# Performance work log

Measured on AMD Instinct MI355X. Metric: run time of the kernel, lower is better.

## Reference

```python
import jax, jax.numpy as jnp
import numpy as np

EMBED = 1024
HEADS = 16
HEAD_DIM = EMBED // HEADS

def setup_inputs() -> dict:
    key = jax.random.key(0)
    ks = jax.random.split(key, 5)
    B, S = 2, 2048
    scale = 1.0 / np.sqrt(EMBED)
    return {
        "query": jax.random.normal(ks[0], (B, S, EMBED), dtype=jnp.float32),
        "w_qkv": jax.random.normal(ks[1], (3 * EMBED, EMBED), dtype=jnp.float32) * scale,
        "b_qkv": jax.random.normal(ks[2], (3 * EMBED,), dtype=jnp.float32) * 0.01,
        "w_out": jax.random.normal(ks[3], (EMBED, EMBED), dtype=jnp.float32) * scale,
        "b_out": jax.random.normal(ks[4], (EMBED,), dtype=jnp.float32) * 0.01,
    }

def reference(query, w_qkv, b_qkv, w_out, b_out):
    B, S, E = query.shape
    H, D = HEADS, HEAD_DIM
    # fused qkv projection (torch Linear: x @ W.T + b)
    qkv = query @ w_qkv.T + b_qkv          # [B, S, 3E]
    q, k, v = jnp.split(qkv, 3, axis=-1)   # each [B, S, E]
    def heads(x):
        return x.reshape(B, S, H, D).transpose(0, 2, 1, 3)  # [B, H, S, D]
    q, k, v = heads(q), heads(k), heads(v)
    scale = D ** -0.5
    energy = jnp.einsum('bhqd,bhkd->bhqk', q, k) * scale    # [B, H, S, S]
    attn = jax.nn.softmax(energy, axis=-1)
    # dropout: inference mode (identity)
    out = jnp.einsum('bhqk,bhkd->bhqd', attn, v)            # [B, H, S, D]
    out = out.transpose(0, 2, 1, 3).reshape(B, S, E)
    return out @ w_out.T + b_out
```

## Files before the change

### kernel.cpp

```cpp
#include <hip/hip_runtime.h>
#include <hip/hip_bf16.h>
#include <cstdint>
#include <cstddef>


typedef float f32x4  __attribute__((ext_vector_type(4)));
typedef float f32x16 __attribute__((ext_vector_type(16)));
typedef short s16x8  __attribute__((ext_vector_type(8)));

#define AS1C(p) ((const __attribute__((address_space(1))) void*)(p))
#define AS3(p)  ((__attribute__((address_space(3))) void*)(p))

__device__ __forceinline__ unsigned short f2bf(float f) {
    union { float f; unsigned u; } v; v.f = f;
    return (unsigned short)((v.u + 0x7FFFu + ((v.u >> 16) & 1u)) >> 16);
}

__device__ __forceinline__ float fast_exp2(float x) {
#if __has_builtin(__builtin_amdgcn_exp2f)
    return __builtin_amdgcn_exp2f(x);
#else
    return exp2f(x);
#endif
}

__device__ __forceinline__ float fast_rcp(float x) {
#if __has_builtin(__builtin_amdgcn_rcpf)
    return __builtin_amdgcn_rcpf(x);
#else
    return 1.0f / x;
#endif
}

__device__ __forceinline__ unsigned pk_bf2(float lo, float hi) {
    __hip_bfloat162 p = __float22bfloat162_rn(make_float2(lo, hi));
    return *(unsigned*)&p;
}

__global__ void cvt_bf16_3(const float* __restrict__ a, const float* __restrict__ b,
                           const float* __restrict__ c,
                           unsigned short* __restrict__ oa, unsigned short* __restrict__ ob,
                           unsigned short* __restrict__ oc,
                           int na4, int nb4, int nc4) {
    int j = blockIdx.x * blockDim.x + threadIdx.x;
    const float* s; unsigned short* d;
    if (j < na4) { s = a; d = oa; }
    else {
        j -= na4;
        if (j < nb4) { s = b; d = ob; }
        else { j -= nb4; if (j >= nc4) return; s = c; d = oc; }
    }
    float4 f = reinterpret_cast<const float4*>(s)[j];
    ushort4 o;
    o.x = f2bf(f.x); o.y = f2bf(f.y); o.z = f2bf(f.z); o.w = f2bf(f.w);
    reinterpret_cast<ushort4*>(d)[j] = o;
}

#define QSCALE_L2E (0.125f * 1.44269504088896f)

template <int MODE>
__global__ __launch_bounds__(256, 2)
void gemm_bt(const unsigned short* __restrict__ A,
             const unsigned short* __restrict__ B,
             const float* __restrict__ bias,
             float* __restrict__ Cf,
             unsigned short* __restrict__ Qw,
             unsigned short* __restrict__ Kw,
             unsigned short* __restrict__ Vtw,
             int M, int N, int K) {
    constexpr int BK = 32;
    __shared__ unsigned short As[128 * BK];
    __shared__ unsigned short Bs[128 * BK];

    const int tid = threadIdx.x;
    const int wid = tid >> 6, lane = tid & 63;
    const int brow = blockIdx.y * 128, bcol = blockIdx.x * 128;
    const int wr = wid >> 1, wc = wid & 1;

    f32x4 acc[4][4] = {};

    const int kIters = K / BK;
    for (int kt = 0; kt < kIters; ++kt) {
#pragma unroll
        for (int i = 0; i < 2; ++i) {
            const int lb = (wid * 2 + i) * 1024;
            const int row = (lb >> 6) + (lane >> 2);
            const int inrow = (lane & 3) * 16;
            const char* ga = (const char*)A + ((size_t)(brow + row) * K + kt * BK) * 2 + inrow;
            __builtin_amdgcn_global_load_lds(AS1C(ga), AS3((char*)As + lb), 16, 0, 0);
            const char* gb = (const char*)B + ((size_t)(bcol + row) * K + kt * BK) * 2 + inrow;
            __builtin_amdgcn_global_load_lds(AS1C(gb), AS3((char*)Bs + lb), 16, 0, 0);
        }
        __syncthreads();

        s16x8 af[4], bfr[4];
#pragma unroll
        for (int f = 0; f < 4; ++f) {
            af[f]  = *(const s16x8*)((const char*)As + (wr * 64 + f * 16 + (lane & 15)) * 64 + (lane >> 4) * 16);
            bfr[f] = *(const s16x8*)((const char*)Bs + (wc * 64 + f * 16 + (lane & 15)) * 64 + (lane >> 4) * 16);
        }
#pragma unroll
        for (int mf = 0; mf < 4; ++mf)
#pragma unroll
            for (int nf = 0; nf < 4; ++nf)
                acc[mf][nf] = __builtin_amdgcn_mfma_f32_16x16x32_bf16(af[mf], bfr[nf], acc[mf][nf], 0, 0, 0);
        __syncthreads();
    }

    float bv[4];
#pragma unroll
    for (int nf = 0; nf < 4; ++nf) bv[nf] = bias[bcol + wc * 64 + nf * 16 + (lane & 15)];

#pragma unroll
    for (int mf = 0; mf < 4; ++mf) {
#pragma unroll
        for (int r = 0; r < 4; ++r) {
            const int row = brow + wr * 64 + mf * 16 + (lane >> 4) * 4 + r;
#pragma unroll
            for (int nf = 0; nf < 4; ++nf) {
                const int col = bcol + wc * 64 + nf * 16 + (lane & 15);
                float v = acc[mf][nf][r] + bv[nf];
                if constexpr (MODE == 0) {
                    const int which = col >> 10, e = col & 1023;
                    const int h = e >> 6, d = e & 63;
                    const int b = row >> 11, s = row & 2047;
                    const size_t bh = (size_t)(b * 16 + h);
                    if (which == 0)      Qw[(bh * 2048 + s) * 64 + d] = f2bf(v * QSCALE_L2E);
                    else if (which == 1) Kw[(bh * 2048 + s) * 64 + d] = f2bf(v);
                    else                 Vtw[(bh * 64 + d) * 2048 + s] = f2bf(v);
                } else {
                    Cf[(size_t)row * N + col] = v;
                }
            }
        }
    }
}

__global__ __launch_bounds__(128, 2)
void attn_fwd(const unsigned short* __restrict__ Q,
              const unsigned short* __restrict__ Kk,
              const unsigned short* __restrict__ Vt,
              unsigned short* __restrict__ O) {
    __shared__ unsigned short Ks[2][64 * 64];
    __shared__ unsigned short Vs[2][64 * 64];

    const int tid = threadIdx.x;
    const int wid = tid >> 6, lane = tid & 63;

    const int bid = blockIdx.x;
    const int swzb = (bid & 7) * 128 + (bid >> 3);
    const int bh = swzb >> 5;
    const int qt = swzb & 31;
    const int b = bh >> 4, h = bh & 15;
    const int q0 = qt * 64 + wid * 32;

    const char* Qb  = (const char*)(Q  + (size_t)bh * 2048 * 64);
    const char* Kb  = (const char*)(Kk + (size_t)bh * 2048 * 64);
    const char* Vtb = (const char*)(Vt + (size_t)bh * 64 * 2048);

    const int x = lane & 31, hh = lane >> 5;

    s16x8 aq[4];
#pragma unroll
    for (int kf = 0; kf < 4; ++kf)
        aq[kf] = *(const s16x8*)(Qb + (size_t)(q0 + x) * 128 + (kf * 16 + hh * 8) * 2);

    f32x16 o_acc[2] = {};
    f32x16 l_acc = {};
    s16x8 ones;
#pragma unroll
    for (int j = 0; j < 8; ++j) ones[j] = (short)0x3F80;

    auto stage = [&](int kc, int buf) {
#pragma unroll
        for (int i = 0; i < 4; ++i) {
            const int s = wid * 4 + i;
            const int row = s * 8 + (lane >> 3);
            const int inrow = ((lane & 7) * 16) ^ ((row & 7) << 4);
            const char* gk = Kb + (size_t)(kc * 64 + row) * 128 + inrow;
            __builtin_amdgcn_global_load_lds(AS1C(gk), AS3((char*)Ks[buf] + s * 1024), 16, 0, 0);
            const char* gv = Vtb + (size_t)row * 4096 + kc * 128 + inrow;
            __builtin_amdgcn_global_load_lds(AS1C(gv), AS3((char*)Vs[buf] + s * 1024), 16, 0, 0);
        }
    };

    stage(0, 0);
    __syncthreads();

    for (int kc = 0; kc < 32; ++kc) {
        const int cur = kc & 1;
        if (kc < 31) stage(kc + 1, cur ^ 1);

        f32x16 sacc[2] = {};
#pragma unroll
        for (int kt2 = 0; kt2 < 2; ++kt2) {
#pragma unroll
            for (int kf = 0; kf < 4; ++kf) {
                const s16x8 bk = *(const s16x8*)((const char*)Ks[cur] + (kt2 * 32 + x) * 128 +
                                                 ((kf * 32 + hh * 16) ^ ((x & 7) << 4)));
                sacc[kt2] = __builtin_amdgcn_mfma_f32_32x32x16_bf16(bk, aq[kf], sacc[kt2], 0, 0, 0);
            }
        }

        unsigned p2x[8], p2y[8];
#pragma unroll
        for (int kt2 = 0; kt2 < 2; ++kt2)
#pragma unroll
            for (int c = 0; c < 4; ++c) {
                p2x[kt2 * 4 + c] = pk_bf2(fast_exp2(sacc[kt2][4 * c + 0]), fast_exp2(sacc[kt2][4 * c + 1]));
                p2y[kt2 * 4 + c] = pk_bf2(fast_exp2(sacc[kt2][4 * c + 2]), fast_exp2(sacc[kt2][4 * c + 3]));
            }

        s16x8 pa[2][2];
#pragma unroll
        for (int kt2 = 0; kt2 < 2; ++kt2)
#pragma unroll
            for (int cp = 0; cp < 2; ++cp) {
                unsigned ax = p2x[kt2 * 4 + 2 * cp], bx = p2x[kt2 * 4 + 2 * cp + 1];
                unsigned ay = p2y[kt2 * 4 + 2 * cp], by = p2y[kt2 * 4 + 2 * cp + 1];
                asm("v_permlane32_swap_b32 %0, %1" : "+v"(ax), "+v"(bx));
                asm("v_permlane32_swap_b32 %0, %1" : "+v"(ay), "+v"(by));
                union { s16x8 v; unsigned u[4]; } u;
                u.u[0] = ax; u.u[1] = ay; u.u[2] = bx; u.u[3] = by;
                pa[kt2][cp] = u.v;
            }

#pragma unroll
        for (int kt2 = 0; kt2 < 2; ++kt2)
#pragma unroll
            for (int cp = 0; cp < 2; ++cp) {
                l_acc = __builtin_amdgcn_mfma_f32_32x32x16_bf16(pa[kt2][cp], ones, l_acc, 0, 0, 0);
#pragma unroll
                for (int dt = 0; dt < 2; ++dt) {
                    const int row = dt * 32 + x;
                    const s16x8 bv = *(const s16x8*)((const char*)Vs[cur] + row * 128 +
                                                     ((kt2 * 64 + cp * 32 + hh * 16) ^ ((x & 7) << 4)));
                    o_acc[dt] = __builtin_amdgcn_mfma_f32_32x32x16_bf16(pa[kt2][cp], bv, o_acc[dt], 0, 0, 0);
                }
            }
        __syncthreads();
    }

    float inv[16];
#pragma unroll
    for (int r = 0; r < 16; ++r) inv[r] = fast_rcp(l_acc[r]);
#pragma unroll
    for (int dt = 0; dt < 2; ++dt) {
#pragma unroll
        for (int r = 0; r < 16; ++r) {
            const int qrow = q0 + (r & 3) + 8 * (r >> 2) + 4 * hh;
            const int d = dt * 32 + x;
            O[(size_t)(b * 2048 + qrow) * 1024 + h * 64 + d] = f2bf(o_acc[dt][r] * inv[r]);
        }
    }
}

extern "C" void kernel_launch(void* const* d_in, const int* in_sizes, int n_in,
                              void* d_out, int out_size, void* d_ws, size_t ws_size,
                              hipStream_t stream) {
    const float* query = (const float*)d_in[0];
    const float* w_qkv = (const float*)d_in[1];
    const float* b_qkv = (const float*)d_in[2];
    const float* w_out = (const float*)d_in[3];
    const float* b_out = (const float*)d_in[4];
    float* out = (float*)d_out;

    unsigned short* ws = (unsigned short*)d_ws;
    unsigned short* Xbf    = ws;
    unsigned short* Wqkvbf = Xbf + 4096 * 1024;
    unsigned short* Woutbf = Wqkvbf + 3072 * 1024;
    unsigned short* Qw     = Woutbf + 1024 * 1024;
    unsigned short* Kw     = Qw + 32 * 2048 * 64;
    unsigned short* Vtw    = Kw + 32 * 2048 * 64;
    unsigned short* Obf    = Vtw + 32 * 2048 * 64;

    const int na4 = 4096 * 1024 / 4, nb4 = 3072 * 1024 / 4, nc4 = 1024 * 1024 / 4;
    cvt_bf16_3<<<(na4 + nb4 + nc4 + 255) / 256, 256, 0, stream>>>(
        query, w_qkv, w_out, Xbf, Wqkvbf, Woutbf, na4, nb4, nc4);

    gemm_bt<0><<<dim3(3072 / 128, 4096 / 128), 256, 0, stream>>>(
        Xbf, Wqkvbf, b_qkv, nullptr, Qw, Kw, Vtw, 4096, 3072, 1024);

    attn_fwd<<<dim3(1024), 128, 0, stream>>>(Qw, Kw, Vtw, Obf);

    gemm_bt<1><<<dim3(1024 / 128, 4096 / 128), 256, 0, stream>>>(
        Obf, Woutbf, b_out, out, nullptr, nullptr, nullptr, 4096, 1024, 1024);
}
```

Before: 135.0 us.

## Load K/V fragments directly from global memory, dropping LDS staging in attention

The attention kernel now runs one wave per block with 32 query rows and reads K and V^T MFMA operands straight from global memory into registers. This removes the shared-memory double buffering, async global-to-LDS loads and per-iteration barriers. In exchange, K/V are no longer shared between two waves, so global/L2 traffic per query row doubles, and global load latency is exposed with no explicit prefetch.

```diff
diff --git a/kernel.cpp b/kernel.cpp
--- a/kernel.cpp
+++ b/kernel.cpp
@@ -136,23 +136,19 @@
     }
 }
 
-__global__ __launch_bounds__(128, 2)
+__global__ __launch_bounds__(64)
 void attn_fwd(const unsigned short* __restrict__ Q,
               const unsigned short* __restrict__ Kk,
               const unsigned short* __restrict__ Vt,
               unsigned short* __restrict__ O) {
-    __shared__ unsigned short Ks[2][64 * 64];
-    __shared__ unsigned short Vs[2][64 * 64];
-
-    const int tid = threadIdx.x;
-    const int wid = tid >> 6, lane = tid & 63;
+    const int lane = threadIdx.x;
 
     const int bid = blockIdx.x;
-    const int swzb = (bid & 7) * 128 + (bid >> 3);
-    const int bh = swzb >> 5;
-    const int qt = swzb & 31;
+    const int swzb = (bid & 7) * 256 + (bid >> 3);
+    const int bh = swzb >> 6;
+    const int qt = swzb & 63;
     const int b = bh >> 4, h = bh & 15;
-    const int q0 = qt * 64 + wid * 32;
+    const int q0 = qt * 32;
 
     const char* Qb  = (const char*)(Q  + (size_t)bh * 2048 * 64);
     const char* Kb  = (const char*)(Kk + (size_t)bh * 2048 * 64);
@@ -171,36 +167,30 @@
 #pragma unroll
     for (int j = 0; j < 8; ++j) ones[j] = (short)0x3F80;
 
-    auto stage = [&](int kc, int buf) {
-#pragma unroll
-        for (int i = 0; i < 4; ++i) {
-            const int s = wid * 4 + i;
-            const int row = s * 8 + (lane >> 3);
-            const int inrow = ((lane & 7) * 16) ^ ((row & 7) << 4);
-            const char* gk = Kb + (size_t)(kc * 64 + row) * 128 + inrow;
-            __builtin_amdgcn_global_load_lds(AS1C(gk), AS3((char*)Ks[buf] + s * 1024), 16, 0, 0);
-            const char* gv = Vtb + (size_t)row * 4096 + kc * 128 + inrow;
-            __builtin_amdgcn_global_load_lds(AS1C(gv), AS3((char*)Vs[buf] + s * 1024), 16, 0, 0);
-        }
-    };
-
-    stage(0, 0);
-    __syncthreads();
-
     for (int kc = 0; kc < 32; ++kc) {
-        const int cur = kc & 1;
-        if (kc < 31) stage(kc + 1, cur ^ 1);
+        s16x8 bk[2][4];
+#pragma unroll
+        for (int kt2 = 0; kt2 < 2; ++kt2)
+#pragma unroll
+            for (int kf = 0; kf < 4; ++kf)
+                bk[kt2][kf] = *(const s16x8*)(Kb + (size_t)(kc * 64 + kt2 * 32 + x) * 128 +
+                                              (kf * 16 + hh * 8) * 2);
+        s16x8 bv[2][2][2];
+#pragma unroll
+        for (int kt2 = 0; kt2 < 2; ++kt2)
+#pragma unroll
+            for (int cp = 0; cp < 2; ++cp)
+#pragma unroll
+                for (int dt = 0; dt < 2; ++dt)
+                    bv[kt2][cp][dt] = *(const s16x8*)(Vtb + (size_t)(dt * 32 + x) * 4096 +
+                                                      (size_t)(kc * 64 + kt2 * 32 + cp * 16 + hh * 8) * 2);
 
         f32x16 sacc[2] = {};
 #pragma unroll
-        for (int kt2 = 0; kt2 < 2; ++kt2) {
-#pragma unroll
-            for (int kf = 0; kf < 4; ++kf) {
-                const s16x8 bk = *(const s16x8*)((const char*)Ks[cur] + (kt2 * 32 + x) * 128 +
-                                                 ((kf * 32 + hh * 16) ^ ((x & 7) << 4)));
-                sacc[kt2] = __builtin_amdgcn_mfma_f32_32x32x16_bf16(bk, aq[kf], sacc[kt2], 0, 0, 0);
-            }
-        }
+        for (int kt2 = 0; kt2 < 2; ++kt2)
+#pragma unroll
+            for (int kf = 0; kf < 4; ++kf)
+                sacc[kt2] = __builtin_amdgcn_mfma_f32_32x32x16_bf16(bk[kt2][kf], aq[kf], sacc[kt2], 0, 0, 0);
 
         unsigned p2x[8], p2y[8];
 #pragma unroll
@@ -231,14 +221,9 @@
             for (int cp = 0; cp < 2; ++cp) {
                 l_acc = __builtin_amdgcn_mfma_f32_32x32x16_bf16(pa[kt2][cp], ones, l_acc, 0, 0, 0);
 #pragma unroll
-                for (int dt = 0; dt < 2; ++dt) {
-                    const int row = dt * 32 + x;
-                    const s16x8 bv = *(const s16x8*)((const char*)Vs[cur] + row * 128 +
-                                                     ((kt2 * 64 + cp * 32 + hh * 16) ^ ((x & 7) << 4)));
-                    o_acc[dt] = __builtin_amdgcn_mfma_f32_32x32x16_bf16(pa[kt2][cp], bv, o_acc[dt], 0, 0, 0);
-                }
-            }
-        __syncthreads();
+                for (int dt = 0; dt < 2; ++dt)
+                    o_acc[dt] = __builtin_amdgcn_mfma_f32_32x32x16_bf16(pa[kt2][cp], bv[kt2][cp][dt], o_acc[dt], 0, 0, 0);
+            }
     }
 
     float inv[16];
@@ -281,7 +266,7 @@
     gemm_bt<0><<<dim3(3072 / 128, 4096 / 128), 256, 0, stream>>>(
         Xbf, Wqkvbf, b_qkv, nullptr, Qw, Kw, Vtw, 4096, 3072, 1024);
 
-    attn_fwd<<<dim3(1024), 128, 0, stream>>>(Qw, Kw, Vtw, Obf);
+    attn_fwd<<<dim3(2048), 64, 0, stream>>>(Qw, Kw, Vtw, Obf);
 
     gemm_bt<1><<<dim3(1024 / 128, 4096 / 128), 256, 0, stream>>>(
         Obf, Woutbf, b_out, out, nullptr, nullptr, nullptr, 4096, 1024, 1024);
```

New measurement: 194.2 us. 43.8% more time.
